# Optimization experiments

Hardware: AMD Instinct MI355X
Metric: run time of the kernel (lower is better)

The kernel has to match this reference:

```python
import jax, jax.numpy as jnp
import numpy as np

VEC_DIM = 64
RANK = 2


def setup_inputs() -> dict:
    key = jax.random.key(0)
    kg, km, kp = jax.random.split(key, 3)
    grid = jax.random.normal(kg, (193, 193, VEC_DIM), dtype=jnp.float32)
    # nn.init.uniform_(M.weight, -0.5, 0.5)
    M_weight = jax.random.uniform(km, (VEC_DIM, VEC_DIM), minval=-0.5, maxval=0.5, dtype=jnp.float32)
    # nn.init.uniform_(P, -0.1, 0.1)
    P = jax.random.uniform(kp, (VEC_DIM, VEC_DIM), minval=-0.1, maxval=0.1, dtype=jnp.float32)
    return {"grid": grid, "M_weight": M_weight, "P": P}


def reference(grid, M_weight, P):
    H, W, m = grid.shape
    # periods1[i,j] = periods2[i,j] = i*m + j + 2
    periods = (jnp.arange(m, dtype=jnp.float32)[:, None] * m
               + jnp.arange(m, dtype=jnp.float32)[None, :] + 2.0)  # [m, m]

    # ---- window extraction: linear mode (step=1), rank_mode='drop', rank_op='avg' ----
    nH = H - RANK + 1
    nW = W - RANK + 1
    win_sum = jax.lax.reduce_window(grid, 0.0, jax.lax.add,
                                    (RANK, RANK, 1), (1, 1, 1), 'VALID')  # [nH, nW, m]
    x_win = (win_sum / float(RANK * RANK)).reshape(nH * nW, m)  # [B, m]

    # ---- map through M (nn.Linear, no bias): y = x @ W^T ----
    x = x_win @ M_weight.T  # [B, m]

    # ---- phi_table gather: phi[k1,k2] = cos(2*pi*k1/periods) * cos(2*pi*k2/periods) ----
    two_pi = jnp.float32(2.0 * np.pi)
    k1s = jnp.arange(nH, dtype=jnp.float32)
    k2s = jnp.arange(nW, dtype=jnp.float32)
    cos1 = jnp.cos(two_pi * k1s[:, None, None] / periods)  # [nH, m, m]
    cos2 = jnp.cos(two_pi * k2s[:, None, None] / periods)  # [nW, m, m]
    phi = (cos1[:, None, :, :] * cos2[None, :, :, :]).reshape(nH * nW, m, m)  # [B, m, m]

    # ---- Nk = einsum('bj,ij,bij->bi', x, P, phi) ----
    Nk = jnp.einsum('bj,ij,bij->bi', x, P, phi)  # [B, m]
    return Nk
```

## Files before the change

kernel.cpp:

```cpp
#include <hip/hip_runtime.h>
#include <math.h>

#define NW 192
#define Wt 193
#define CHUNK 48
#define NMAIN 768

__device__ __forceinline__ float cos_revr(float num, float rcpden) {
    float rev = num * rcpden;
    rev = __builtin_amdgcn_fractf(rev);
    return __builtin_amdgcn_cosf(rev);
}

__global__ __launch_bounds__(512, 4) void k_fused(const float* __restrict__ grid,
                                                  const float* __restrict__ Mw,
                                                  const float* __restrict__ P,
                                                  float* __restrict__ out) {
    __shared__ float bufA[4096];
    __shared__ float bufB[4096];
    __shared__ float xls[CHUNK * 68];

    int bx = blockIdx.x;
    int k1  = bx >> 2;
    int k2s = (bx & 3) * CHUNK;
    int t = threadIdx.x;
    int lane = t & 63;
    int w = __builtin_amdgcn_readfirstlane(t >> 6);
    int jb = w * 8;

    #pragma unroll
    for (int r = 0; r < 2; ++r)
        ((float4*)bufB)[r * 512 + t] = ((const float4*)Mw)[r * 512 + t];
    {
        int c = lane;
        const float* gb  = grid + ((size_t)k1 * Wt + k2s) * 64 + c;
        const float* gb1 = gb + (size_t)Wt * 64;
        #pragma unroll
        for (int r = 0; r < 6; ++r) {
            int p = w * 6 + r;
            float s = gb[p * 64] + gb[(p + 1) * 64]
                    + gb1[p * 64] + gb1[(p + 1) * 64];
            bufA[p * 68 + c] = 0.25f * s;
        }
    }
    __syncthreads();

    if (lane < CHUNK) {
        float accj[8];
        #pragma unroll
        for (int r = 0; r < 8; ++r) accj[r] = 0.f;
        #pragma unroll
        for (int q4 = 0; q4 < 4; ++q4) {
            float4 wv0 = *(const float4*)&bufA[lane * 68 + q4 * 16];
            float4 wv1 = *(const float4*)&bufA[lane * 68 + q4 * 16 + 4];
            float4 wv2 = *(const float4*)&bufA[lane * 68 + q4 * 16 + 8];
            float4 wv3 = *(const float4*)&bufA[lane * 68 + q4 * 16 + 12];
            #pragma unroll
            for (int r = 0; r < 8; ++r) {
                const float4* mrow = (const float4*)&bufB[(jb + r) * 64 + q4 * 16];
                float4 m0 = mrow[0], m1 = mrow[1], m2 = mrow[2], m3 = mrow[3];
                accj[r] += wv0.x * m0.x + wv0.y * m0.y + wv0.z * m0.z + wv0.w * m0.w
                         + wv1.x * m1.x + wv1.y * m1.y + wv1.z * m1.z + wv1.w * m1.w
                         + wv2.x * m2.x + wv2.y * m2.y + wv2.z * m2.z + wv2.w * m2.w
                         + wv3.x * m3.x + wv3.y * m3.y + wv3.z * m3.z + wv3.w * m3.w;
            }
        }
        #pragma unroll
        for (int r = 0; r < 8; ++r)
            xls[lane * 68 + jb + r] = accj[r];
    }
    __syncthreads();

    {
        const float4* P4 = (const float4*)P;
        #pragma unroll
        for (int s = 0; s < 2; ++s) {
            int e = s * 512 + t;
            float4 v = P4[e];
            int i = e >> 4, j0 = (e & 15) * 4;
            bufA[(j0 + 0) * 64 + i] = v.x;
            bufA[(j0 + 1) * 64 + i] = v.y;
            bufA[(j0 + 2) * 64 + i] = v.z;
            bufA[(j0 + 3) * 64 + i] = v.w;
        }
    }
    __syncthreads();

    float A[8], c1v[8], ce[8], co[8];
    #pragma unroll
    for (int jl = 0; jl < 8; ++jl) {
        float T  = (float)(lane * 64 + jb + jl + 2);
        float rT = __builtin_amdgcn_rcpf(T);
        A[jl]   = 2.0f * cos_revr(1.0f, rT);
        c1v[jl] = cos_revr((float)k1, rT) * bufA[(jb + jl) * 64 + lane];
        ce[jl]  = cos_revr((float)k2s, rT);
        co[jl]  = cos_revr((float)(k2s - 1), rT);
    }
    float* part = bufB;

    #pragma unroll
    for (int sub = 0; sub < 6; ++sub) {
        #pragma unroll
        for (int m = 0; m < 4; ++m) {
            {
                int k2i = sub * 8 + 2 * m;
                const float4* xq = (const float4*)&xls[k2i * 68 + jb];
                float4 q0 = xq[0], q1 = xq[1];
                float xs[8] = {q0.x, q0.y, q0.z, q0.w, q1.x, q1.y, q1.z, q1.w};
                float pa = 0.f, pb = 0.f;
                #pragma unroll
                for (int jl = 0; jl < 4; ++jl) {
                    pa     = fmaf(xs[jl] * c1v[jl], ce[jl], pa);
                    co[jl] = fmaf(A[jl], ce[jl], -co[jl]);
                }
                #pragma unroll
                for (int jl = 4; jl < 8; ++jl) {
                    pb     = fmaf(xs[jl] * c1v[jl], ce[jl], pb);
                    co[jl] = fmaf(A[jl], ce[jl], -co[jl]);
                }
                part[(w * 8 + 2 * m) * 64 + lane] = pa + pb;
            }
            {
                int k2i = sub * 8 + 2 * m + 1;
                const float4* xq = (const float4*)&xls[k2i * 68 + jb];
                float4 q0 = xq[0], q1 = xq[1];
                float xs[8] = {q0.x, q0.y, q0.z, q0.w, q1.x, q1.y, q1.z, q1.w};
                float pa = 0.f, pb = 0.f;
                #pragma unroll
                for (int jl = 0; jl < 4; ++jl) {
                    pa     = fmaf(xs[jl] * c1v[jl], co[jl], pa);
                    ce[jl] = fmaf(A[jl], co[jl], -ce[jl]);
                }
                #pragma unroll
                for (int jl = 4; jl < 8; ++jl) {
                    pb     = fmaf(xs[jl] * c1v[jl], co[jl], pb);
                    ce[jl] = fmaf(A[jl], co[jl], -ce[jl]);
                }
                part[(w * 8 + 2 * m + 1) * 64 + lane] = pa + pb;
            }
        }
        __syncthreads();
        {
            int k2l = t >> 6, i = t & 63;
            float r = 0.f;
            #pragma unroll
            for (int ww = 0; ww < 8; ++ww)
                r += part[ww * 512 + k2l * 64 + i];
            out[((size_t)k1 * NW + (k2s + sub * 8 + k2l)) * 64 + i] = r;
        }
        __syncthreads();
    }
}

extern "C" void kernel_launch(void* const* d_in, const int* in_sizes, int n_in,
                              void* d_out, int out_size, void* d_ws, size_t ws_size,
                              hipStream_t stream) {
    const float* grid = (const float*)d_in[0];
    const float* Mw   = (const float*)d_in[1];
    const float* P    = (const float*)d_in[2];
    float* out = (float*)d_out;
    (void)d_ws; (void)ws_size;

    k_fused<<<NMAIN, 512, 0, stream>>>(grid, Mw, P, out);
}
```

Before: 94.30 us.

## Keep projected window vectors in registers and broadcast via readlane

```diff
diff --git a/kernel.cpp b/kernel.cpp
--- a/kernel.cpp
+++ b/kernel.cpp
@@ -12,13 +12,16 @@
     return __builtin_amdgcn_cosf(rev);
 }
 
+__device__ __forceinline__ float rdlane(float v, int l) {
+    return __builtin_bit_cast(float,
+        __builtin_amdgcn_readlane(__builtin_bit_cast(int, v), l));
+}
+
 __global__ __launch_bounds__(512, 4) void k_fused(const float* __restrict__ grid,
                                                   const float* __restrict__ Mw,
                                                   const float* __restrict__ P,
                                                   float* __restrict__ out) {
-    __shared__ float bufA[4096];
-    __shared__ float bufB[4096];
-    __shared__ float xls[CHUNK * 68];
+    __shared__ float part[4096];
 
     int bx = blockIdx.x;
     int k1  = bx >> 2;
@@ -28,125 +31,96 @@
     int w = __builtin_amdgcn_readfirstlane(t >> 6);
     int jb = w * 8;
 
+    float accj[8];
     #pragma unroll
-    for (int r = 0; r < 2; ++r)
-        ((float4*)bufB)[r * 512 + t] = ((const float4*)Mw)[r * 512 + t];
+    for (int r = 0; r < 8; ++r) accj[r] = 0.f;
     {
-        int c = lane;
-        const float* gb  = grid + ((size_t)k1 * Wt + k2s) * 64 + c;
-        const float* gb1 = gb + (size_t)Wt * 64;
+        int p = lane < CHUNK ? lane : CHUNK - 1;
+        const float* g00 = grid + ((size_t)k1 * Wt + k2s + p) * 64;
+        const float* g10 = g00 + (size_t)Wt * 64;
         #pragma unroll
-        for (int r = 0; r < 6; ++r) {
-            int p = w * 6 + r;
-            float s = gb[p * 64] + gb[(p + 1) * 64]
-                    + gb1[p * 64] + gb1[(p + 1) * 64];
-            bufA[p * 68 + c] = 0.25f * s;
+        for (int q = 0; q < 16; ++q) {
+            float4 a = *(const float4*)(g00 + 4 * q);
+            float4 b = *(const float4*)(g00 + 64 + 4 * q);
+            float4 c = *(const float4*)(g10 + 4 * q);
+            float4 d = *(const float4*)(g10 + 64 + 4 * q);
+            float4 w4;
+            w4.x = 0.25f * (a.x + b.x + c.x + d.x);
+            w4.y = 0.25f * (a.y + b.y + c.y + d.y);
+            w4.z = 0.25f * (a.z + b.z + c.z + d.z);
+            w4.w = 0.25f * (a.w + b.w + c.w + d.w);
+            #pragma unroll
+            for (int r = 0; r < 8; ++r) {
+                const float4 m = *(const float4*)&Mw[(jb + r) * 64 + 4 * q];
+                accj[r] += w4.x * m.x + w4.y * m.y + w4.z * m.z + w4.w * m.w;
+            }
         }
     }
-    __syncthreads();
 
-    if (lane < CHUNK) {
-        float accj[8];
+    float A[8], ce[8], co[8];
+    {
+        float4 pr0 = *(const float4*)&P[lane * 64 + jb];
+        float4 pr1 = *(const float4*)&P[lane * 64 + jb + 4];
+        float pv[8] = {pr0.x, pr0.y, pr0.z, pr0.w, pr1.x, pr1.y, pr1.z, pr1.w};
+        float k1f = (float)k1, k2f = (float)k2s;
         #pragma unroll
-        for (int r = 0; r < 8; ++r) accj[r] = 0.f;
-        #pragma unroll
-        for (int q4 = 0; q4 < 4; ++q4) {
-            float4 wv0 = *(const float4*)&bufA[lane * 68 + q4 * 16];
-            float4 wv1 = *(const float4*)&bufA[lane * 68 + q4 * 16 + 4];
-            float4 wv2 = *(const float4*)&bufA[lane * 68 + q4 * 16 + 8];
-            float4 wv3 = *(const float4*)&bufA[lane * 68 + q4 * 16 + 12];
-            #pragma unroll
-            for (int r = 0; r < 8; ++r) {
-                const float4* mrow = (const float4*)&bufB[(jb + r) * 64 + q4 * 16];
-                float4 m0 = mrow[0], m1 = mrow[1], m2 = mrow[2], m3 = mrow[3];
-                accj[r] += wv0.x * m0.x + wv0.y * m0.y + wv0.z * m0.z + wv0.w * m0.w
-                         + wv1.x * m1.x + wv1.y * m1.y + wv1.z * m1.z + wv1.w * m1.w
-                         + wv2.x * m2.x + wv2.y * m2.y + wv2.z * m2.z + wv2.w * m2.w
-                         + wv3.x * m3.x + wv3.y * m3.y + wv3.z * m3.z + wv3.w * m3.w;
-            }
-        }
-        #pragma unroll
-        for (int r = 0; r < 8; ++r)
-            xls[lane * 68 + jb + r] = accj[r];
-    }
-    __syncthreads();
-
-    {
-        const float4* P4 = (const float4*)P;
-        #pragma unroll
-        for (int s = 0; s < 2; ++s) {
-            int e = s * 512 + t;
-            float4 v = P4[e];
-            int i = e >> 4, j0 = (e & 15) * 4;
-            bufA[(j0 + 0) * 64 + i] = v.x;
-            bufA[(j0 + 1) * 64 + i] = v.y;
-            bufA[(j0 + 2) * 64 + i] = v.z;
-            bufA[(j0 + 3) * 64 + i] = v.w;
+        for (int jl = 0; jl < 8; ++jl) {
+            float T  = (float)(lane * 64 + jb + jl + 2);
+            float rT = __builtin_amdgcn_rcpf(T);
+            A[jl]    = 2.0f * cos_revr(1.0f, rT);
+            float c1 = cos_revr(k1f, rT) * pv[jl];
+            ce[jl]   = cos_revr(k2f, rT) * c1;
+            co[jl]   = cos_revr(k2f - 1.0f, rT) * c1;
         }
     }
-    __syncthreads();
-
-    float A[8], c1v[8], ce[8], co[8];
-    #pragma unroll
-    for (int jl = 0; jl < 8; ++jl) {
-        float T  = (float)(lane * 64 + jb + jl + 2);
-        float rT = __builtin_amdgcn_rcpf(T);
-        A[jl]   = 2.0f * cos_revr(1.0f, rT);
-        c1v[jl] = cos_revr((float)k1, rT) * bufA[(jb + jl) * 64 + lane];
-        ce[jl]  = cos_revr((float)k2s, rT);
-        co[jl]  = cos_revr((float)(k2s - 1), rT);
-    }
-    float* part = bufB;
 
     #pragma unroll
     for (int sub = 0; sub < 6; ++sub) {
         #pragma unroll
         for (int m = 0; m < 4; ++m) {
             {
-                int k2i = sub * 8 + 2 * m;
-                const float4* xq = (const float4*)&xls[k2i * 68 + jb];
-                float4 q0 = xq[0], q1 = xq[1];
-                float xs[8] = {q0.x, q0.y, q0.z, q0.w, q1.x, q1.y, q1.z, q1.w};
+                int s = 2 * m;
+                int k2i = sub * 8 + s;
                 float pa = 0.f, pb = 0.f;
                 #pragma unroll
                 for (int jl = 0; jl < 4; ++jl) {
-                    pa     = fmaf(xs[jl] * c1v[jl], ce[jl], pa);
+                    float xs = rdlane(accj[jl], k2i);
+                    pa     = fmaf(xs, ce[jl], pa);
                     co[jl] = fmaf(A[jl], ce[jl], -co[jl]);
                 }
                 #pragma unroll
                 for (int jl = 4; jl < 8; ++jl) {
-                    pb     = fmaf(xs[jl] * c1v[jl], ce[jl], pb);
+                    float xs = rdlane(accj[jl], k2i);
+                    pb     = fmaf(xs, ce[jl], pb);
                     co[jl] = fmaf(A[jl], ce[jl], -co[jl]);
                 }
-                part[(w * 8 + 2 * m) * 64 + lane] = pa + pb;
+                part[(w * 8 + s) * 64 + lane] = pa + pb;
             }
             {
-                int k2i = sub * 8 + 2 * m + 1;
-                const float4* xq = (const float4*)&xls[k2i * 68 + jb];
-                float4 q0 = xq[0], q1 = xq[1];
-                float xs[8] = {q0.x, q0.y, q0.z, q0.w, q1.x, q1.y, q1.z, q1.w};
+                int s = 2 * m + 1;
+                int k2i = sub * 8 + s;
                 float pa = 0.f, pb = 0.f;
                 #pragma unroll
                 for (int jl = 0; jl < 4; ++jl) {
-                    pa     = fmaf(xs[jl] * c1v[jl], co[jl], pa);
+                    float xs = rdlane(accj[jl], k2i);
+                    pa     = fmaf(xs, co[jl], pa);
                     ce[jl] = fmaf(A[jl], co[jl], -ce[jl]);
                 }
                 #pragma unroll
                 for (int jl = 4; jl < 8; ++jl) {
-                    pb     = fmaf(xs[jl] * c1v[jl], co[jl], pb);
+                    float xs = rdlane(accj[jl], k2i);
+                    pb     = fmaf(xs, co[jl], pb);
                     ce[jl] = fmaf(A[jl], co[jl], -ce[jl]);
                 }
-                part[(w * 8 + 2 * m + 1) * 64 + lane] = pa + pb;
+                part[(w * 8 + s) * 64 + lane] = pa + pb;
             }
         }
         __syncthreads();
         {
-            int k2l = t >> 6, i = t & 63;
-            float r = 0.f;
+            float r = part[t];
             #pragma unroll
-            for (int ww = 0; ww < 8; ++ww)
-                r += part[ww * 512 + k2l * 64 + i];
-            out[((size_t)k1 * NW + (k2s + sub * 8 + k2l)) * 64 + i] = r;
+            for (int ww = 1; ww < 8; ++ww) r += part[ww * 512 + t];
+            out[((size_t)k1 * NW + (k2s + sub * 8 + (t >> 6))) * 64 + (t & 63)] = r;
         }
         __syncthreads();
     }
```

Result: slower. 107.8 us (+14.4%).
